# Optimization experiments

Measured on AMD Instinct MI355X. Metric: run time of the kernel, lower is better.

## Reference

```python
import jax, jax.numpy as jnp
import numpy as np

# Module hyperparameters (from init_kwargs)
N, C, L = 8, 256, 8192
K = 3            # kernel_size
G = 8            # groups
GC = C // G      # group channels = 32
PAD = 1
DIL = 1
OFFSET_SCALE = 1.0
LN_EPS = 1e-6


def setup_inputs() -> dict:
    key = jax.random.key(0)
    k1, k2, k3, k4, k5 = jax.random.split(key, 5)
    x = jax.random.normal(k1, (N, C, L), dtype=jnp.float32)
    # LayerNorm affine params
    ln_w = 1.0 + 0.1 * jax.random.normal(k2, (C,), dtype=jnp.float32)
    ln_b = 0.1 * jax.random.normal(k3, (C,), dtype=jnp.float32)
    # offset/mask linear: C -> G*K*2 (zero-init in the module; small random here
    # so the deformable sampling path is exercised non-trivially)
    om_w = 0.02 * jax.random.normal(k4, (G * K * 2, C), dtype=jnp.float32)
    om_b = 0.02 * jax.random.normal(k5, (G * K * 2,), dtype=jnp.float32)
    return {"x": x, "ln_w": ln_w, "ln_b": ln_b, "om_w": om_w, "om_b": om_b}


def _dcnv4_1d(x, ln_w, ln_b, om_w, om_b):
    # x: [N, C, L]
    xt = jnp.transpose(x, (0, 2, 1))                       # [N, L, C]
    # LayerNorm over channels
    mu = xt.mean(-1, keepdims=True)
    var = xt.var(-1, keepdims=True)
    xn = (xt - mu) * jax.lax.rsqrt(var + LN_EPS) * ln_w + ln_b
    xa = jax.nn.gelu(xn, approximate=False)                # [N, L, C]

    # offset / mask projection
    om = jnp.einsum('nlc,oc->nlo', xa, om_w) + om_b        # [N, L, 2*G*K]
    off = om[..., : G * K].reshape(N, L, G, K)             # [N, L, G, K]
    mask = om[..., G * K:].reshape(N, L, G, K)             # [N, L, G, K]

    # sampling positions: conv grid + learned offsets
    base = (jnp.arange(L, dtype=jnp.float32)[:, None] - PAD
            + DIL * jnp.arange(K, dtype=jnp.float32)[None, :])   # [L, K]
    p = base[None, :, None, :] + OFFSET_SCALE * off        # [N, L, G, K]

    p0 = jnp.floor(p)
    w1 = p - p0                                            # linear interp weight
    w0 = 1.0 - w1
    i0 = p0.astype(jnp.int32)
    i1 = i0 + 1
    v0 = ((i0 >= 0) & (i0 < L)).astype(x.dtype)
    v1 = ((i1 >= 0) & (i1 < L)).astype(x.dtype)
    w0 = w0 * v0
    w1 = w1 * v1
    i0c = jnp.clip(i0, 0, L - 1)
    i1c = jnp.clip(i1, 0, L - 1)

    # group the features: [N, G, GC, L]
    xg = jnp.transpose(xa.reshape(N, L, G, GC), (0, 2, 3, 1))

    def gather(idx):  # idx: [N, L, G, K] -> values [N, G, GC, L, K]
        it = jnp.transpose(idx, (0, 2, 1, 3)).reshape(N, G, 1, L * K)
        it = jnp.broadcast_to(it, (N, G, GC, L * K))
        return jnp.take_along_axis(xg, it, axis=3).reshape(N, G, GC, L, K)

    samp = gather(i0c) * jnp.transpose(w0, (0, 2, 1, 3))[:, :, None] \
         + gather(i1c) * jnp.transpose(w1, (0, 2, 1, 3))[:, :, None]  # [N,G,GC,L,K]

    # mask-weighted aggregation over kernel taps (DCNv4: raw mask, no softmax)
    out = jnp.einsum('ngclk,nlgk->ngcl', samp, mask)       # [N, G, GC, L]
    return out.reshape(N, C, L)


def reference(x, ln_w, ln_b, om_w, om_b):
    return _dcnv4_1d(x, ln_w, ln_b, om_w, om_b)
```

## Files before the change

### kernel.cpp

```cpp
#include <hip/hip_runtime.h>
#include <hip/hip_bf16.h>
#include <math.h>

#define NN 8
#define CC 256
#define LL 8192
#define KK 3
#define GG 8
#define GCC 32
#define OMD 48
#define TILE_L 128
#define TL 32

typedef __attribute__((ext_vector_type(8))) short short8v;
typedef __attribute__((ext_vector_type(4))) float floatx4;

__device__ inline ushort f2bf(float f) {
    uint u = __float_as_uint(f);
    u += 0x7fffu + ((u >> 16) & 1u);
    return (ushort)(u >> 16);
}

__device__ inline float gelu_fast(float xn) {
    float u = xn * xn;
    float z = xn * (-1.5957691216f - 0.0713548162726f * u);
    return __fdividef(xn, 1.f + __expf(z));
}

__global__ __launch_bounds__(256, 6) void k_ln_gelu(
    const float* __restrict__ x,
    const float* __restrict__ ln_w, const float* __restrict__ ln_b,
    __hip_bfloat16* __restrict__ xa)
{
    __shared__ float xs[128 * 33];
    int n  = blockIdx.y;
    int l0 = blockIdx.x * TL;
    int t  = threadIdx.x;
    int p   = t >> 3;
    int sub = t & 7;
    int pp  = p ^ (sub << 2);

    const float* xbase = x + (size_t)n * CC * LL + l0;
    float r[32];

    float4 v[8];
    #pragma unroll
    for (int it = 0; it < 8; ++it) {
        int idx = it * 256 + t;
        int c   = idx >> 3;
        int l4  = idx & 7;
        v[it] = *reinterpret_cast<const float4*>(xbase + (size_t)c * LL + l4 * 4);
    }

    #pragma unroll
    for (int half = 0; half < 2; ++half) {
        if (half) __syncthreads();
        #pragma unroll
        for (int it = 0; it < 4; ++it) {
            int idx = (half * 4 + it) * 256 + t;
            int cl  = (idx >> 3) & 127;
            int l4  = idx & 7;
            int sw  = (cl >> 4) << 2;
            int b   = cl * 33;
            float4 vv = v[half * 4 + it];
            xs[b + ((4 * l4 + 0) ^ sw)] = vv.x;
            xs[b + ((4 * l4 + 1) ^ sw)] = vv.y;
            xs[b + ((4 * l4 + 2) ^ sw)] = vv.z;
            xs[b + ((4 * l4 + 3) ^ sw)] = vv.w;
        }
        __syncthreads();
        #pragma unroll
        for (int j = 0; j < 16; ++j)
            r[half * 16 + j] = xs[(sub * 16 + j) * 33 + pp];
    }

    float sum = 0.f, sq = 0.f;
    #pragma unroll
    for (int j = 0; j < 32; ++j) { sum += r[j]; sq = fmaf(r[j], r[j], sq); }
    #pragma unroll
    for (int m = 1; m <= 4; m <<= 1) {
        sum += __shfl_xor(sum, m);
        sq  += __shfl_xor(sq, m);
    }
    float mean = sum * (1.f / 256.f);
    float rstd = rsqrtf(sq * (1.f / 256.f) - mean * mean + 1e-6f);

    __hip_bfloat16* xarow = xa + ((size_t)n * LL + l0 + p) * CC;
    #pragma unroll
    for (int half = 0; half < 2; ++half) {
        int cb = half * 128 + sub * 16;
        ushort pk[16];
        #pragma unroll
        for (int q = 0; q < 4; ++q) {
            float4 lw = *reinterpret_cast<const float4*>(ln_w + cb + 4 * q);
            float4 lb = *reinterpret_cast<const float4*>(ln_b + cb + 4 * q);
            float lww[4] = {lw.x, lw.y, lw.z, lw.w};
            float lbb[4] = {lb.x, lb.y, lb.z, lb.w};
            #pragma unroll
            for (int i = 0; i < 4; ++i) {
                int j = 4 * q + i;
                float xn = (r[half * 16 + j] - mean) * rstd * lww[i] + lbb[i];
                pk[j] = f2bf(gelu_fast(xn));
            }
        }
        uint4* dst = reinterpret_cast<uint4*>(xarow + cb);
        #pragma unroll
        for (int q = 0; q < 2; ++q) {
            uint4 w4;
            w4.x = (uint)pk[8*q+0] | ((uint)pk[8*q+1] << 16);
            w4.y = (uint)pk[8*q+2] | ((uint)pk[8*q+3] << 16);
            w4.z = (uint)pk[8*q+4] | ((uint)pk[8*q+5] << 16);
            w4.w = (uint)pk[8*q+6] | ((uint)pk[8*q+7] << 16);
            dst[q] = w4;
        }
    }
}

__global__ __launch_bounds__(256, 4) void k_om_mfma(
    const __hip_bfloat16* __restrict__ xa, const float* __restrict__ om_w,
    const float* __restrict__ om_b, float* __restrict__ om)
{
    __shared__ __align__(16) ushort wL[12288];

    int t    = threadIdx.x;
    #pragma unroll
    for (int it = 0; it < 48; ++it) {
        int idx = it * 256 + t;
        int o   = idx >> 8;
        int c   = idx & 255;
        int nt  = o >> 4;
        int ks  = c >> 5;
        int qq  = (c & 31) >> 3;
        int j   = c & 7;
        int lane = (o & 15) | (qq << 4);
        wL[((ks * 3 + nt) * 64 + lane) * 8 + j] = f2bf(om_w[idx]);
    }
    __syncthreads();

    int lane = t & 63;
    int col  = lane & 15;
    int q    = lane >> 4;
    size_t pos0 = ((size_t)blockIdx.x * 8 + (t >> 6) * 2) * 16;

    const ushort* xp = reinterpret_cast<const ushort*>(xa);
    const short8v* A0 = reinterpret_cast<const short8v*>(xp + (pos0 + col) * CC + q * 8);
    const short8v* A1 = reinterpret_cast<const short8v*>(xp + (pos0 + 16 + col) * CC + q * 8);
    const short8v* Bb = reinterpret_cast<const short8v*>(wL) + lane;

    floatx4 c00 = {0.f,0.f,0.f,0.f}, c01 = {0.f,0.f,0.f,0.f}, c02 = {0.f,0.f,0.f,0.f};
    floatx4 c10 = {0.f,0.f,0.f,0.f}, c11 = {0.f,0.f,0.f,0.f}, c12 = {0.f,0.f,0.f,0.f};
    #pragma unroll
    for (int ks = 0; ks < 8; ++ks) {
        short8v a0 = A0[ks * 4];
        short8v a1 = A1[ks * 4];
        short8v b0 = Bb[(ks * 3 + 0) * 64];
        short8v b1 = Bb[(ks * 3 + 1) * 64];
        short8v b2 = Bb[(ks * 3 + 2) * 64];
        c00 = __builtin_amdgcn_mfma_f32_16x16x32_bf16(a0, b0, c00, 0, 0, 0);
        c10 = __builtin_amdgcn_mfma_f32_16x16x32_bf16(a1, b0, c10, 0, 0, 0);
        c01 = __builtin_amdgcn_mfma_f32_16x16x32_bf16(a0, b1, c01, 0, 0, 0);
        c11 = __builtin_amdgcn_mfma_f32_16x16x32_bf16(a1, b1, c11, 0, 0, 0);
        c02 = __builtin_amdgcn_mfma_f32_16x16x32_bf16(a0, b2, c02, 0, 0, 0);
        c12 = __builtin_amdgcn_mfma_f32_16x16x32_bf16(a1, b2, c12, 0, 0, 0);
    }
    float b0 = om_b[col];
    float b1 = om_b[16 + col];
    float b2 = om_b[32 + col];
    {
        float* d = om + (pos0 + q * 4) * OMD + col;
        #pragma unroll
        for (int i = 0; i < 4; ++i) {
            d[(size_t)i * OMD]      = c00[i] + b0;
            d[(size_t)i * OMD + 16] = c01[i] + b1;
            d[(size_t)i * OMD + 32] = c02[i] + b2;
        }
    }
    {
        float* d = om + (pos0 + 16 + q * 4) * OMD + col;
        #pragma unroll
        for (int i = 0; i < 4; ++i) {
            d[(size_t)i * OMD]      = c10[i] + b0;
            d[(size_t)i * OMD + 16] = c11[i] + b1;
            d[(size_t)i * OMD + 32] = c12[i] + b2;
        }
    }
}

__global__ __launch_bounds__(256) void k_dcn(
    const __hip_bfloat16* __restrict__ xa, const float* __restrict__ om,
    float* __restrict__ out)
{
    int lt = blockIdx.x, g = blockIdx.y, n = blockIdx.z;
    int l0 = lt * TILE_L;

    __shared__ int   i0_s[TILE_L * KK];
    __shared__ int   i1_s[TILE_L * KK];
    __shared__ float w0_s[TILE_L * KK];
    __shared__ float w1_s[TILE_L * KK];
    __shared__ float out_s[GCC][TILE_L + 4];

    int t = threadIdx.x;

    for (int idx = t; idx < TILE_L * KK; idx += 256) {
        int ll = idx / KK, k = idx - KK * (idx / KK);
        int l = l0 + ll;
        const float* omp = om + ((size_t)n * LL + l) * OMD;
        float off  = omp[g * KK + k];
        float mask = omp[GG * KK + g * KK + k];
        float p  = (float)(l - 1 + k) + off;
        float p0 = floorf(p);
        float w1 = p - p0;
        float w0 = 1.f - w1;
        int i0 = (int)p0;
        int i1 = i0 + 1;
        float ws0 = (i0 >= 0 && i0 < LL) ? mask * w0 : 0.f;
        float ws1 = (i1 >= 0 && i1 < LL) ? mask * w1 : 0.f;
        i0_s[idx] = min(max(i0, 0), LL - 1);
        i1_s[idx] = min(max(i1, 0), LL - 1);
        w0_s[idx] = ws0;
        w1_s[idx] = ws1;
    }
    __syncthreads();

    int cq = t & 3;
    int ps = t >> 2;
    const __hip_bfloat16* xab = xa + (size_t)n * LL * CC + g * GCC + cq * 8;

    #pragma unroll
    for (int it = 0; it < 2; ++it) {
        int ll = it * 64 + ps;
        float acc[8] = {0.f,0.f,0.f,0.f,0.f,0.f,0.f,0.f};
        #pragma unroll
        for (int k = 0; k < KK; ++k) {
            int idx = ll * KK + k;
            int i0 = i0_s[idx];
            int i1 = i1_s[idx];
            float a0 = w0_s[idx];
            float a1 = w1_s[idx];
            uint4 r0 = *reinterpret_cast<const uint4*>(xab + (size_t)i0 * CC);
            uint4 r1 = *reinterpret_cast<const uint4*>(xab + (size_t)i1 * CC);
            uint u0[4] = {r0.x, r0.y, r0.z, r0.w};
            uint u1[4] = {r1.x, r1.y, r1.z, r1.w};
            #pragma unroll
            for (int d = 0; d < 4; ++d) {
                acc[2*d]   = fmaf(a0, __uint_as_float(u0[d] << 16),
                             fmaf(a1, __uint_as_float(u1[d] << 16), acc[2*d]));
                acc[2*d+1] = fmaf(a0, __uint_as_float(u0[d] & 0xffff0000u),
                             fmaf(a1, __uint_as_float(u1[d] & 0xffff0000u), acc[2*d+1]));
            }
        }
        #pragma unroll
        for (int j = 0; j < 8; ++j) out_s[cq * 8 + j][ll] = acc[j];
    }
    __syncthreads();

    int c4 = t & 31;
    int rw = t >> 5;
    float* op = out + ((size_t)n * CC + (size_t)g * GCC) * LL + l0;
    #pragma unroll
    for (int rr = 0; rr < 4; ++rr) {
        int row = rw + rr * 8;
        float4 vv = *reinterpret_cast<const float4*>(&out_s[row][c4 * 4]);
        *reinterpret_cast<float4*>(op + (size_t)row * LL + c4 * 4) = vv;
    }
}

extern "C" void kernel_launch(void* const* d_in, const int* in_sizes, int n_in,
                              void* d_out, int out_size, void* d_ws, size_t ws_size,
                              hipStream_t stream) {
    const float* x    = (const float*)d_in[0];
    const float* ln_w = (const float*)d_in[1];
    const float* ln_b = (const float*)d_in[2];
    const float* om_w = (const float*)d_in[3];
    const float* om_b = (const float*)d_in[4];
    float* out = (float*)d_out;

    __hip_bfloat16* xa = (__hip_bfloat16*)((char*)d_ws + 49152);
    float* om = (float*)((char*)d_ws + 49152 + (size_t)NN * LL * CC * 2);

    dim3 g1a(LL / TL, NN);
    k_ln_gelu<<<g1a, 256, 0, stream>>>(x, ln_w, ln_b, xa);

    k_om_mfma<<<512, 256, 0, stream>>>(xa, om_w, om_b, om);

    dim3 grid2(LL / TILE_L, GG, NN);
    k_dcn<<<grid2, 256, 0, stream>>>(xa, om, out);
}
```

Before: 56.12 us.

## Fuse offset/mask projection into deformable sampling kernel via shared memory

Merges the MFMA offset/mask projection kernel and the deformable gather kernel into a single kernel. Each block handles 64 positions for one batch and keeps the 48-wide projection result in shared memory instead of writing it to global memory and reading it back. The block then loops over all 8 groups, computing sampling indices and weights on the fly. This removes one launch and the om round trip. In exchange each block reconverts the full weight matrix to shared memory, syncs twice per group, has fewer blocks (1024), and lowers the occupancy bound from 4 to 3.

Result: faster. 54.32 us (-3.2%).

```diff
diff --git a/kernel.cpp b/kernel.cpp
--- a/kernel.cpp
+++ b/kernel.cpp
@@ -9,8 +9,8 @@
 #define GG 8
 #define GCC 32
 #define OMD 48
-#define TILE_L 128
 #define TL 32
+#define FT 64
 
 typedef __attribute__((ext_vector_type(8))) short short8v;
 typedef __attribute__((ext_vector_type(4))) float floatx4;
@@ -116,13 +116,18 @@
     }
 }
 
-__global__ __launch_bounds__(256, 4) void k_om_mfma(
+__global__ __launch_bounds__(256, 3) void k_fused(
     const __hip_bfloat16* __restrict__ xa, const float* __restrict__ om_w,
-    const float* __restrict__ om_b, float* __restrict__ om)
+    const float* __restrict__ om_b, float* __restrict__ out)
 {
     __shared__ __align__(16) ushort wL[12288];
-
-    int t    = threadIdx.x;
+    __shared__ float om_s[FT * 49];
+    __shared__ float out_s[GCC][68];
+
+    int t  = threadIdx.x;
+    int n  = blockIdx.y;
+    int l0 = blockIdx.x * FT;
+
     #pragma unroll
     for (int it = 0; it < 48; ++it) {
         int idx = it * 256 + t;
@@ -138,105 +143,57 @@
     __syncthreads();
 
     int lane = t & 63;
+    int wv   = t >> 6;
     int col  = lane & 15;
     int q    = lane >> 4;
-    size_t pos0 = ((size_t)blockIdx.x * 8 + (t >> 6) * 2) * 16;
-
     const ushort* xp = reinterpret_cast<const ushort*>(xa);
-    const short8v* A0 = reinterpret_cast<const short8v*>(xp + (pos0 + col) * CC + q * 8);
-    const short8v* A1 = reinterpret_cast<const short8v*>(xp + (pos0 + 16 + col) * CC + q * 8);
+    const short8v* A0 = reinterpret_cast<const short8v*>(
+        xp + ((size_t)n * LL + l0 + wv * 16 + col) * CC + q * 8);
     const short8v* Bb = reinterpret_cast<const short8v*>(wL) + lane;
 
-    floatx4 c00 = {0.f,0.f,0.f,0.f}, c01 = {0.f,0.f,0.f,0.f}, c02 = {0.f,0.f,0.f,0.f};
-    floatx4 c10 = {0.f,0.f,0.f,0.f}, c11 = {0.f,0.f,0.f,0.f}, c12 = {0.f,0.f,0.f,0.f};
+    floatx4 c0 = {0.f,0.f,0.f,0.f}, c1 = {0.f,0.f,0.f,0.f}, c2 = {0.f,0.f,0.f,0.f};
     #pragma unroll
     for (int ks = 0; ks < 8; ++ks) {
-        short8v a0 = A0[ks * 4];
-        short8v a1 = A1[ks * 4];
-        short8v b0 = Bb[(ks * 3 + 0) * 64];
-        short8v b1 = Bb[(ks * 3 + 1) * 64];
-        short8v b2 = Bb[(ks * 3 + 2) * 64];
-        c00 = __builtin_amdgcn_mfma_f32_16x16x32_bf16(a0, b0, c00, 0, 0, 0);
-        c10 = __builtin_amdgcn_mfma_f32_16x16x32_bf16(a1, b0, c10, 0, 0, 0);
-        c01 = __builtin_amdgcn_mfma_f32_16x16x32_bf16(a0, b1, c01, 0, 0, 0);
-        c11 = __builtin_amdgcn_mfma_f32_16x16x32_bf16(a1, b1, c11, 0, 0, 0);
-        c02 = __builtin_amdgcn_mfma_f32_16x16x32_bf16(a0, b2, c02, 0, 0, 0);
-        c12 = __builtin_amdgcn_mfma_f32_16x16x32_bf16(a1, b2, c12, 0, 0, 0);
+        short8v a = A0[ks * 4];
+        c0 = __builtin_amdgcn_mfma_f32_16x16x32_bf16(a, Bb[(ks*3+0)*64], c0, 0, 0, 0);
+        c1 = __builtin_amdgcn_mfma_f32_16x16x32_bf16(a, Bb[(ks*3+1)*64], c1, 0, 0, 0);
+        c2 = __builtin_amdgcn_mfma_f32_16x16x32_bf16(a, Bb[(ks*3+2)*64], c2, 0, 0, 0);
     }
     float b0 = om_b[col];
     float b1 = om_b[16 + col];
     float b2 = om_b[32 + col];
-    {
-        float* d = om + (pos0 + q * 4) * OMD + col;
-        #pragma unroll
-        for (int i = 0; i < 4; ++i) {
-            d[(size_t)i * OMD]      = c00[i] + b0;
-            d[(size_t)i * OMD + 16] = c01[i] + b1;
-            d[(size_t)i * OMD + 32] = c02[i] + b2;
-        }
-    }
-    {
-        float* d = om + (pos0 + 16 + q * 4) * OMD + col;
-        #pragma unroll
-        for (int i = 0; i < 4; ++i) {
-            d[(size_t)i * OMD]      = c10[i] + b0;
-            d[(size_t)i * OMD + 16] = c11[i] + b1;
-            d[(size_t)i * OMD + 32] = c12[i] + b2;
-        }
-    }
-}
-
-__global__ __launch_bounds__(256) void k_dcn(
-    const __hip_bfloat16* __restrict__ xa, const float* __restrict__ om,
-    float* __restrict__ out)
-{
-    int lt = blockIdx.x, g = blockIdx.y, n = blockIdx.z;
-    int l0 = lt * TILE_L;
-
-    __shared__ int   i0_s[TILE_L * KK];
-    __shared__ int   i1_s[TILE_L * KK];
-    __shared__ float w0_s[TILE_L * KK];
-    __shared__ float w1_s[TILE_L * KK];
-    __shared__ float out_s[GCC][TILE_L + 4];
-
-    int t = threadIdx.x;
-
-    for (int idx = t; idx < TILE_L * KK; idx += 256) {
-        int ll = idx / KK, k = idx - KK * (idx / KK);
-        int l = l0 + ll;
-        const float* omp = om + ((size_t)n * LL + l) * OMD;
-        float off  = omp[g * KK + k];
-        float mask = omp[GG * KK + g * KK + k];
-        float p  = (float)(l - 1 + k) + off;
-        float p0 = floorf(p);
-        float w1 = p - p0;
-        float w0 = 1.f - w1;
-        int i0 = (int)p0;
-        int i1 = i0 + 1;
-        float ws0 = (i0 >= 0 && i0 < LL) ? mask * w0 : 0.f;
-        float ws1 = (i1 >= 0 && i1 < LL) ? mask * w1 : 0.f;
-        i0_s[idx] = min(max(i0, 0), LL - 1);
-        i1_s[idx] = min(max(i1, 0), LL - 1);
-        w0_s[idx] = ws0;
-        w1_s[idx] = ws1;
+    #pragma unroll
+    for (int i = 0; i < 4; ++i) {
+        int row = wv * 16 + q * 4 + i;
+        om_s[row * 49 + col]      = c0[i] + b0;
+        om_s[row * 49 + 16 + col] = c1[i] + b1;
+        om_s[row * 49 + 32 + col] = c2[i] + b2;
     }
     __syncthreads();
 
     int cq = t & 3;
     int ps = t >> 2;
-    const __hip_bfloat16* xab = xa + (size_t)n * LL * CC + g * GCC + cq * 8;
-
-    #pragma unroll
-    for (int it = 0; it < 2; ++it) {
-        int ll = it * 64 + ps;
+    int c4 = t & 15;
+    int rw = t >> 4;
+    size_t xb2 = (size_t)n * LL * CC;
+
+    for (int g = 0; g < GG; ++g) {
+        const __hip_bfloat16* xab = xa + xb2 + g * GCC + cq * 8;
         float acc[8] = {0.f,0.f,0.f,0.f,0.f,0.f,0.f,0.f};
         #pragma unroll
         for (int k = 0; k < KK; ++k) {
-            int idx = ll * KK + k;
-            int i0 = i0_s[idx];
-            int i1 = i1_s[idx];
-            float a0 = w0_s[idx];
-            float a1 = w1_s[idx];
+            float off  = om_s[ps * 49 + g * KK + k];
+            float mask = om_s[ps * 49 + 24 + g * KK + k];
+            float p  = (float)(l0 + ps - 1 + k) + off;
+            float p0 = floorf(p);
+            float w1 = p - p0;
+            float w0 = 1.f - w1;
+            int i0 = (int)p0;
+            int i1 = i0 + 1;
+            float a0 = (i0 >= 0 && i0 < LL) ? mask * w0 : 0.f;
+            float a1 = (i1 >= 0 && i1 < LL) ? mask * w1 : 0.f;
+            i0 = min(max(i0, 0), LL - 1);
+            i1 = min(max(i1, 0), LL - 1);
             uint4 r0 = *reinterpret_cast<const uint4*>(xab + (size_t)i0 * CC);
             uint4 r1 = *reinterpret_cast<const uint4*>(xab + (size_t)i1 * CC);
             uint u0[4] = {r0.x, r0.y, r0.z, r0.w};
@@ -250,18 +207,17 @@
             }
         }
         #pragma unroll
-        for (int j = 0; j < 8; ++j) out_s[cq * 8 + j][ll] = acc[j];
-    }
-    __syncthreads();
-
-    int c4 = t & 31;
-    int rw = t >> 5;
-    float* op = out + ((size_t)n * CC + (size_t)g * GCC) * LL + l0;
-    #pragma unroll
-    for (int rr = 0; rr < 4; ++rr) {
-        int row = rw + rr * 8;
-        float4 vv = *reinterpret_cast<const float4*>(&out_s[row][c4 * 4]);
-        *reinterpret_cast<float4*>(op + (size_t)row * LL + c4 * 4) = vv;
+        for (int j = 0; j < 8; ++j) out_s[cq * 8 + j][ps] = acc[j];
+        __syncthreads();
+
+        float* op = out + ((size_t)n * CC + (size_t)g * GCC) * LL + l0;
+        #pragma unroll
+        for (int rr = 0; rr < 2; ++rr) {
+            int row = rw + rr * 16;
+            float4 vv = *reinterpret_cast<const float4*>(&out_s[row][c4 * 4]);
+            *reinterpret_cast<float4*>(op + (size_t)row * LL + c4 * 4) = vv;
+        }
+        __syncthreads();
     }
 }
 
@@ -276,13 +232,10 @@
     float* out = (float*)d_out;
 
     __hip_bfloat16* xa = (__hip_bfloat16*)((char*)d_ws + 49152);
-    float* om = (float*)((char*)d_ws + 49152 + (size_t)NN * LL * CC * 2);
-
-    dim3 g1a(LL / TL, NN);
-    k_ln_gelu<<<g1a, 256, 0, stream>>>(x, ln_w, ln_b, xa);
-
-    k_om_mfma<<<512, 256, 0, stream>>>(xa, om_w, om_b, om);
-
-    dim3 grid2(LL / TILE_L, GG, NN);
-    k_dcn<<<grid2, 256, 0, stream>>>(xa, om, out);
-}
+
+    dim3 g1(LL / TL, NN);
+    k_ln_gelu<<<g1, 256, 0, stream>>>(x, ln_w, ln_b, xa);
+
+    dim3 g2(LL / FT, NN);
+    k_fused<<<g2, 256, 0, stream>>>(xa, om_w, om_b, out);
+}
```
